# Kernel optimization log

Measured on AMD Instinct MI355X. Metric: run time of the kernel, lower is better.

The kernel has to match this reference:

```python
import jax, jax.numpy as jnp
import numpy as np

SR = 24000
N_FFT = 1024
N_MELS = 128
FMIN = 0.0
LPC_ORDER = 4
REPEAT = 256
F0 = 40.0
CLAMP = 1e-12
T_FRAMES = 16384


def _hz_to_mel(f):
    # librosa slaney scale
    f = np.asarray(f, dtype=np.float64)
    f_sp = 200.0 / 3
    min_log_hz = 1000.0
    min_log_mel = min_log_hz / f_sp
    logstep = np.log(6.4) / 27.0
    mels = f / f_sp
    log_t = f >= min_log_hz
    mels = np.where(log_t, min_log_mel + np.log(np.maximum(f, min_log_hz) / min_log_hz) / logstep, mels)
    return mels


def _mel_to_hz(m):
    m = np.asarray(m, dtype=np.float64)
    f_sp = 200.0 / 3
    min_log_hz = 1000.0
    min_log_mel = min_log_hz / f_sp
    logstep = np.log(6.4) / 27.0
    freqs = f_sp * m
    log_t = m >= min_log_mel
    freqs = np.where(log_t, min_log_hz * np.exp(logstep * (m - min_log_mel)), freqs)
    return freqs


def librosa_mel_fn(sr, n_fft, n_mels, fmin, fmax):
    if fmax is None:
        fmax = sr / 2.0
    fftfreqs = np.linspace(0.0, sr / 2.0, n_fft // 2 + 1)
    mel_f = _mel_to_hz(np.linspace(_hz_to_mel(fmin), _hz_to_mel(fmax), n_mels + 2))
    fdiff = np.diff(mel_f)
    ramps = mel_f[:, None] - fftfreqs[None, :]
    lower = -ramps[:-2] / fdiff[:-1, None]
    upper = ramps[2:] / fdiff[1:, None]
    weights = np.maximum(0.0, np.minimum(lower, upper))
    enorm = 2.0 / (mel_f[2 : n_mels + 2] - mel_f[:n_mels])  # slaney norm
    weights *= enorm[:, None]
    return weights.astype(np.float32)


def setup_inputs() -> dict:
    key = jax.random.key(0)
    mel = jax.random.normal(key, (1, N_MELS, T_FRAMES), dtype=jnp.float32)
    mel_basis = librosa_mel_fn(SR, N_FFT, N_MELS, FMIN, None)  # [128, 513]
    inv_mel_basis = jnp.asarray(np.linalg.pinv(mel_basis), dtype=jnp.float32)  # [513, 128]
    theta = (2.0 * np.pi * F0 / SR) ** 2
    lag_window = jnp.asarray(
        np.exp(-0.5 * theta * np.arange(LPC_ORDER + 1, dtype=np.float32) ** 2)[:, None],
        dtype=jnp.float32,
    )  # [lpc_order+1, 1]
    return {"mel": mel, "inv_mel_basis": inv_mel_basis, "lag_window": lag_window}


def _levinson_durbin(AC, n):
    # AC: [n+1, T] autocorrelation; returns LPC coeffs [n, T]
    E = AC[0]
    lp = []  # list of [T]
    for i in range(n):
        acc = AC[i + 1]
        for j in range(i):
            acc = acc + lp[j] * AC[i - j]
        ki = acc / E
        c = jnp.maximum(1.0 - ki * ki, 1e-5)
        E = E * c
        lp = [lp[j] - ki * lp[i - j - 1] for j in range(i)] + [-ki]
    return jnp.stack(lp, axis=0)  # [n, T]


def reference(mel, inv_mel_basis, lag_window):
    # mel: [1, n_mel, T]
    mel_lin = jnp.power(10.0, mel)
    linear = jnp.maximum(jnp.einsum("fm,bmt->bft", inv_mel_basis, mel_lin), CLAMP)  # [1, 513, T]
    power = linear ** 2
    flipped = jnp.flip(power, axis=1)[:, 1:-1, :]
    fft_power = jnp.concatenate([power, flipped], axis=1)  # [1, n_fft, T]
    auto_corr = jnp.fft.ifft(fft_power, axis=1).real[:, : LPC_ORDER + 1, :]  # [1, n+1, T]
    auto_corr = auto_corr * lag_window[None, :, :]
    lpc = _levinson_durbin(auto_corr[0], LPC_ORDER)[None]  # [1, n, T]
    lpc_ctrl = -jnp.flip(lpc, axis=1)
    lpc_ctrl = jnp.repeat(lpc_ctrl, REPEAT, axis=-1)  # [1, n, T*repeat]
    return lpc_ctrl
```

## Files before the change

### kernel.cpp

```cpp
#include <hip/hip_runtime.h>

#define T_FRAMES 16384
#define N_MELS 128
#define N_FREQ 513
#define FPB 64
#define BT 512
#define LOG2_10 3.3219280948873623f

typedef short bf16x8 __attribute__((ext_vector_type(8)));
typedef unsigned short u16x8 __attribute__((ext_vector_type(8)));
typedef float f32x4 __attribute__((ext_vector_type(4)));

__device__ __forceinline__ unsigned short f2bf(float x) {
  unsigned u = __float_as_uint(x);
  return (unsigned short)((u + 0x7FFFu + ((u >> 16) & 1u)) >> 16);
}
__device__ __forceinline__ float bf2f(unsigned short h) {
  return __uint_as_float(((unsigned)h) << 16);
}

__global__ __launch_bounds__(256) void build_bimg(
    const float* __restrict__ B, unsigned short* __restrict__ img) {
  int gid = blockIdx.x * 256 + threadIdx.x;
  int l  = gid & 63;
  int hl = (gid >> 6) & 1;
  int ks = (gid >> 7) & 3;
  int ft = (gid >> 9) & 3;
  int w  = gid >> 11;
  int f  = w * 64 + ft * 16 + (l & 15);
  int k0 = ks * 32 + (l >> 4) * 8;
  const float* src = B + f * N_MELS + k0;
  u16x8 o;
#pragma unroll
  for (int j = 0; j < 8; ++j) {
    float x = src[j];
    unsigned short hi = f2bf(x);
    o[j] = hl ? f2bf(x - bf2f(hi)) : hi;
  }
  *((u16x8*)img + gid) = o;
}

__global__ __launch_bounds__(BT, 2) void mel2lpc_mfma(
    const float* __restrict__ mel,
    const float* __restrict__ B,
    const float* __restrict__ lag,
    const unsigned short* __restrict__ bimg,
    float* __restrict__ lpcw)
{
  __shared__ float X32T[64][132];
  __shared__ __align__(16) short Xf[32][512];
  __shared__ float W_s[5][N_FREQ];
  __shared__ float red[8][5][64];

  const int tid = threadIdx.x;
  const int lane = tid & 63;
  const int w = __builtin_amdgcn_readfirstlane(tid >> 6);
  const int t0 = blockIdx.x * FPB;

  for (int idx = tid; idx < 5 * N_FREQ; idx += BT) {
    int k = idx / N_FREQ;
    int f = idx - k * N_FREQ;
    float cf = (f == 0 || f == N_FREQ - 1) ? (1.0f / 1024.0f) : (2.0f / 1024.0f);
    W_s[k][f] = lag[k] * cf * cospif((float)(k * f) * (1.0f / 512.0f));
  }
#pragma unroll
  for (int r = 0; r < 16; ++r) {
    int idx = r * BT + tid;
    int t = idx & 63;
    int m = idx >> 6;
    X32T[t][m] = exp2f(mel[m * T_FRAMES + t0 + t] * LOG2_10);
  }
  __syncthreads();

#pragma unroll
  for (int pi = 0; pi < 2; ++pi) {
    int pr = w * 2 + pi;
    int tt = pr >> 2, ks = pr & 3;
    int t = tt * 16 + (lane & 15);
    int k0 = ks * 32 + (lane >> 4) * 8;
    float4 a0 = *(const float4*)&X32T[t][k0];
    float4 a1 = *(const float4*)&X32T[t][k0 + 4];
    float xs[8] = {a0.x, a0.y, a0.z, a0.w, a1.x, a1.y, a1.z, a1.w};
    u16x8 vh, vl;
#pragma unroll
    for (int j = 0; j < 8; ++j) {
      unsigned short hi = f2bf(xs[j]);
      vh[j] = hi;
      vl[j] = f2bf(xs[j] - bf2f(hi));
    }
    int fi = (tt * 4 + ks) * 2;
    *(u16x8*)&Xf[fi][lane * 8] = vh;
    *(u16x8*)&Xf[fi + 1][lane * 8] = vl;
  }
  __syncthreads();

  f32x4 acc[4][4];
#pragma unroll
  for (int ft = 0; ft < 4; ++ft)
#pragma unroll
    for (int tt = 0; tt < 4; ++tt) acc[ft][tt] = (f32x4){0.f, 0.f, 0.f, 0.f};

  const bf16x8* bfr = (const bf16x8*)bimg;
#pragma unroll
  for (int ks = 0; ks < 4; ++ks) {
    bf16x8 xh[4], xl[4], ah[4], al[4];
#pragma unroll
    for (int tt = 0; tt < 4; ++tt) {
      xh[tt] = *(const bf16x8*)&Xf[(tt * 4 + ks) * 2][lane * 8];
      xl[tt] = *(const bf16x8*)&Xf[(tt * 4 + ks) * 2 + 1][lane * 8];
    }
#pragma unroll
    for (int ft = 0; ft < 4; ++ft) {
      int fr = ((w * 4 + ft) * 4 + ks) * 2;
      ah[ft] = bfr[fr * 64 + lane];
      al[ft] = bfr[(fr + 1) * 64 + lane];
    }
#pragma unroll
    for (int ft = 0; ft < 4; ++ft)
#pragma unroll
      for (int tt = 0; tt < 4; ++tt) {
        acc[ft][tt] = __builtin_amdgcn_mfma_f32_16x16x32_bf16(ah[ft], xh[tt], acc[ft][tt], 0, 0, 0);
        acc[ft][tt] = __builtin_amdgcn_mfma_f32_16x16x32_bf16(ah[ft], xl[tt], acc[ft][tt], 0, 0, 0);
        acc[ft][tt] = __builtin_amdgcn_mfma_f32_16x16x32_bf16(al[ft], xh[tt], acc[ft][tt], 0, 0, 0);
      }
  }

  float pk[5][4];
#pragma unroll
  for (int k = 0; k < 5; ++k)
#pragma unroll
    for (int tt = 0; tt < 4; ++tt) pk[k][tt] = 0.f;

#pragma unroll
  for (int ft = 0; ft < 4; ++ft) {
#pragma unroll
    for (int j = 0; j < 4; ++j) {
      int f = w * 64 + ft * 16 + ((lane >> 4) << 2) + j;
      float w0 = W_s[0][f], w1 = W_s[1][f], w2 = W_s[2][f];
      float w3 = W_s[3][f], w4 = W_s[4][f];
#pragma unroll
      for (int tt = 0; tt < 4; ++tt) {
        float lin = fmaxf(acc[ft][tt][j], 1e-12f);
        float p = lin * lin;
        pk[0][tt] = fmaf(w0, p, pk[0][tt]);
        pk[1][tt] = fmaf(w1, p, pk[1][tt]);
        pk[2][tt] = fmaf(w2, p, pk[2][tt]);
        pk[3][tt] = fmaf(w3, p, pk[3][tt]);
        pk[4][tt] = fmaf(w4, p, pk[4][tt]);
      }
    }
  }
#pragma unroll
  for (int k = 0; k < 5; ++k)
#pragma unroll
    for (int tt = 0; tt < 4; ++tt) {
      float v = pk[k][tt];
      v += __shfl_xor(v, 16);
      v += __shfl_xor(v, 32);
      if (lane < 16) red[w][k][tt * 16 + lane] = v;
    }
  __syncthreads();

  if (tid < 64) {
    const int t = tid;
    float ac[5];
#pragma unroll
    for (int k = 0; k < 5; ++k) {
      float s = 0.f;
#pragma unroll
      for (int w2 = 0; w2 < 8; ++w2) s += red[w2][k][t];
      ac[k] = s;
    }
    float s = 0.f;
    const float4* __restrict__ B512 = (const float4*)(B + 512 * N_MELS);
#pragma unroll
    for (int mi = 0; mi < 32; ++mi) {
      float4 b = B512[mi];
      float4 xv = *(const float4*)&X32T[t][mi * 4];
      s = fmaf(b.x, xv.x, s); s = fmaf(b.y, xv.y, s);
      s = fmaf(b.z, xv.z, s); s = fmaf(b.w, xv.w, s);
    }
    float lin = fmaxf(s, 1e-12f);
    float pv = lin * lin;
#pragma unroll
    for (int k = 0; k < 5; ++k) ac[k] = fmaf(W_s[k][512], pv, ac[k]);

    float E = ac[0];
    float k0 = ac[1] / E;
    E *= fmaxf(1.0f - k0 * k0, 1e-5f);
    float l0 = -k0;

    float a1 = ac[2] + l0 * ac[1];
    float k1 = a1 / E;
    E *= fmaxf(1.0f - k1 * k1, 1e-5f);
    float m0 = l0 - k1 * l0;
    float m1 = -k1;

    float a2 = ac[3] + m0 * ac[2] + m1 * ac[1];
    float k2 = a2 / E;
    E *= fmaxf(1.0f - k2 * k2, 1e-5f);
    float n0 = m0 - k2 * m1;
    float n1 = m1 - k2 * m0;
    float n2 = -k2;

    float a3 = ac[4] + n0 * ac[3] + n1 * ac[2] + n2 * ac[1];
    float k3 = a3 / E;
    float o0 = n0 - k3 * n2;
    float o1 = n1 - k3 * n1;
    float o2 = n2 - k3 * n0;
    float o3 = -k3;

    lpcw[0 * T_FRAMES + t0 + t] = -o3;
    lpcw[1 * T_FRAMES + t0 + t] = -o2;
    lpcw[2 * T_FRAMES + t0 + t] = -o1;
    lpcw[3 * T_FRAMES + t0 + t] = -o0;
  }
}

__global__ __launch_bounds__(256) void expand(
    const float* __restrict__ lpc, float4* __restrict__ out4) {
  int g = blockIdx.x * 2048 + threadIdx.x;
#pragma unroll
  for (int i = 0; i < 8; ++i) {
    int gi = g + i * 256;
    int j = gi >> 20;
    int rem = gi & 1048575;
    int frame = rem >> 6;
    float v = lpc[j * T_FRAMES + frame];
    out4[gi] = make_float4(v, v, v, v);
  }
}

extern "C" void kernel_launch(void* const* d_in, const int* in_sizes, int n_in,
                              void* d_out, int out_size, void* d_ws, size_t ws_size,
                              hipStream_t stream) {
  const float* mel = (const float*)d_in[0];
  const float* B   = (const float*)d_in[1];
  const float* lag = (const float*)d_in[2];
  float* ws = (float*)d_ws;
  unsigned short* bimg = (unsigned short*)ws;
  float* lpcw = ws + 65536;
  build_bimg<<<64, 256, 0, stream>>>(B, bimg);
  mel2lpc_mfma<<<T_FRAMES / FPB, BT, 0, stream>>>(mel, B, lag, bimg, lpcw);
  expand<<<2048, 256, 0, stream>>>(lpcw, (float4*)d_out);
}
```

Before: 97.53 us.

## Fuse repeat-expansion into mel2lpc kernel and halve frames per block

Removes the separate expand kernel: each block now writes its repeated LPC output (4 x 32 frames x 256) directly from shared memory, so the intermediate LPC workspace round trip and one launch go away. Frames per block drop from 64 to 32, shared memory is overlaid into one aliased buffer, and launch bounds are raised to allow 4 blocks per SM, which doubles the grid and raises occupancy. The bin-512 dot product moves earlier so it runs alongside the bf16 split. In exchange, each block reloads the bf16 B image for half as many frames, which doubles B traffic per frame.

```diff
diff --git a/kernel.cpp b/kernel.cpp
--- a/kernel.cpp
+++ b/kernel.cpp
@@ -3,7 +3,7 @@
 #define T_FRAMES 16384
 #define N_MELS 128
 #define N_FREQ 513
-#define FPB 64
+#define FPB 32
 #define BT 512
 #define LOG2_10 3.3219280948873623f
 
@@ -40,42 +40,67 @@
   *((u16x8*)img + gid) = o;
 }
 
-__global__ __launch_bounds__(BT, 2) void mel2lpc_mfma(
+#define SM_X32T 0
+#define SM_RED  0
+#define SM_LP   5120
+#define SM_XF   16896
+#define SM_W    33280
+#define SM_PV   43552
+#define SM_SIZE 43712
+
+__global__ __launch_bounds__(BT, 4) void mel2lpc_mfma(
     const float* __restrict__ mel,
     const float* __restrict__ B,
     const float* __restrict__ lag,
     const unsigned short* __restrict__ bimg,
-    float* __restrict__ lpcw)
+    float* __restrict__ out)
 {
-  __shared__ float X32T[64][132];
-  __shared__ __align__(16) short Xf[32][512];
-  __shared__ float W_s[5][N_FREQ];
-  __shared__ float red[8][5][64];
+  __shared__ __align__(16) char smem[SM_SIZE];
+  float (*X32T)[132] = (float(*)[132])(smem + SM_X32T);
+  short (*Xf)[512]   = (short(*)[512])(smem + SM_XF);
+  float (*W_s)[513]  = (float(*)[513])(smem + SM_W);
+  float (*red)[5][32] = (float(*)[5][32])(smem + SM_RED);
+  float (*lp)[32]    = (float(*)[32])(smem + SM_LP);
+  float* pv512       = (float*)(smem + SM_PV);
 
   const int tid = threadIdx.x;
   const int lane = tid & 63;
   const int w = __builtin_amdgcn_readfirstlane(tid >> 6);
   const int t0 = blockIdx.x * FPB;
 
-  for (int idx = tid; idx < 5 * N_FREQ; idx += BT) {
-    int k = idx / N_FREQ;
-    int f = idx - k * N_FREQ;
-    float cf = (f == 0 || f == N_FREQ - 1) ? (1.0f / 1024.0f) : (2.0f / 1024.0f);
-    W_s[k][f] = lag[k] * cf * cospif((float)(k * f) * (1.0f / 512.0f));
-  }
-#pragma unroll
-  for (int r = 0; r < 16; ++r) {
+#pragma unroll
+  for (int k = 0; k < 5; ++k) {
+    float lk = lag[k];
+    for (int f = tid; f < N_FREQ; f += BT) {
+      float cf = (f == 0 || f == N_FREQ - 1) ? (1.0f / 1024.0f) : (2.0f / 1024.0f);
+      W_s[k][f] = lk * cf * cospif((float)(k * f) * (1.0f / 512.0f));
+    }
+  }
+#pragma unroll
+  for (int r = 0; r < 8; ++r) {
     int idx = r * BT + tid;
-    int t = idx & 63;
-    int m = idx >> 6;
+    int t = idx & 31;
+    int m = idx >> 5;
     X32T[t][m] = exp2f(mel[m * T_FRAMES + t0 + t] * LOG2_10);
   }
   __syncthreads();
 
-#pragma unroll
-  for (int pi = 0; pi < 2; ++pi) {
-    int pr = w * 2 + pi;
-    int tt = pr >> 2, ks = pr & 3;
+  if (tid < FPB) {
+    const int t = tid;
+    float s = 0.f;
+    const float4* __restrict__ B512 = (const float4*)(B + 512 * N_MELS);
+#pragma unroll
+    for (int mi = 0; mi < 32; ++mi) {
+      float4 b = B512[mi];
+      float4 xv = *(const float4*)&X32T[t][mi * 4];
+      s = fmaf(b.x, xv.x, s); s = fmaf(b.y, xv.y, s);
+      s = fmaf(b.z, xv.z, s); s = fmaf(b.w, xv.w, s);
+    }
+    float lin = fmaxf(s, 1e-12f);
+    pv512[t] = lin * lin;
+  }
+  {
+    int tt = w >> 2, ks = w & 3;
     int t = tt * 16 + (lane & 15);
     int k0 = ks * 32 + (lane >> 4) * 8;
     float4 a0 = *(const float4*)&X32T[t][k0];
@@ -88,48 +113,43 @@
       vh[j] = hi;
       vl[j] = f2bf(xs[j] - bf2f(hi));
     }
-    int fi = (tt * 4 + ks) * 2;
-    *(u16x8*)&Xf[fi][lane * 8] = vh;
-    *(u16x8*)&Xf[fi + 1][lane * 8] = vl;
-  }
-  __syncthreads();
-
-  f32x4 acc[4][4];
+    *(u16x8*)&Xf[w * 2][lane * 8] = vh;
+    *(u16x8*)&Xf[w * 2 + 1][lane * 8] = vl;
+  }
+  __syncthreads();
+
+  f32x4 acc[4][2];
 #pragma unroll
   for (int ft = 0; ft < 4; ++ft)
 #pragma unroll
-    for (int tt = 0; tt < 4; ++tt) acc[ft][tt] = (f32x4){0.f, 0.f, 0.f, 0.f};
+    for (int tt = 0; tt < 2; ++tt) acc[ft][tt] = (f32x4){0.f, 0.f, 0.f, 0.f};
 
   const bf16x8* bfr = (const bf16x8*)bimg;
 #pragma unroll
   for (int ks = 0; ks < 4; ++ks) {
-    bf16x8 xh[4], xl[4], ah[4], al[4];
-#pragma unroll
-    for (int tt = 0; tt < 4; ++tt) {
-      xh[tt] = *(const bf16x8*)&Xf[(tt * 4 + ks) * 2][lane * 8];
-      xl[tt] = *(const bf16x8*)&Xf[(tt * 4 + ks) * 2 + 1][lane * 8];
-    }
+    bf16x8 xh0 = *(const bf16x8*)&Xf[(0 * 4 + ks) * 2][lane * 8];
+    bf16x8 xl0 = *(const bf16x8*)&Xf[(0 * 4 + ks) * 2 + 1][lane * 8];
+    bf16x8 xh1 = *(const bf16x8*)&Xf[(1 * 4 + ks) * 2][lane * 8];
+    bf16x8 xl1 = *(const bf16x8*)&Xf[(1 * 4 + ks) * 2 + 1][lane * 8];
 #pragma unroll
     for (int ft = 0; ft < 4; ++ft) {
       int fr = ((w * 4 + ft) * 4 + ks) * 2;
-      ah[ft] = bfr[fr * 64 + lane];
-      al[ft] = bfr[(fr + 1) * 64 + lane];
-    }
-#pragma unroll
-    for (int ft = 0; ft < 4; ++ft)
-#pragma unroll
-      for (int tt = 0; tt < 4; ++tt) {
-        acc[ft][tt] = __builtin_amdgcn_mfma_f32_16x16x32_bf16(ah[ft], xh[tt], acc[ft][tt], 0, 0, 0);
-        acc[ft][tt] = __builtin_amdgcn_mfma_f32_16x16x32_bf16(ah[ft], xl[tt], acc[ft][tt], 0, 0, 0);
-        acc[ft][tt] = __builtin_amdgcn_mfma_f32_16x16x32_bf16(al[ft], xh[tt], acc[ft][tt], 0, 0, 0);
-      }
-  }
-
-  float pk[5][4];
+      bf16x8 ah = bfr[fr * 64 + lane];
+      bf16x8 al = bfr[(fr + 1) * 64 + lane];
+      acc[ft][0] = __builtin_amdgcn_mfma_f32_16x16x32_bf16(ah, xh0, acc[ft][0], 0, 0, 0);
+      acc[ft][0] = __builtin_amdgcn_mfma_f32_16x16x32_bf16(ah, xl0, acc[ft][0], 0, 0, 0);
+      acc[ft][0] = __builtin_amdgcn_mfma_f32_16x16x32_bf16(al, xh0, acc[ft][0], 0, 0, 0);
+      acc[ft][1] = __builtin_amdgcn_mfma_f32_16x16x32_bf16(ah, xh1, acc[ft][1], 0, 0, 0);
+      acc[ft][1] = __builtin_amdgcn_mfma_f32_16x16x32_bf16(ah, xl1, acc[ft][1], 0, 0, 0);
+      acc[ft][1] = __builtin_amdgcn_mfma_f32_16x16x32_bf16(al, xh1, acc[ft][1], 0, 0, 0);
+    }
+  }
+
+  float pk[5][2];
 #pragma unroll
   for (int k = 0; k < 5; ++k)
 #pragma unroll
-    for (int tt = 0; tt < 4; ++tt) pk[k][tt] = 0.f;
+    for (int tt = 0; tt < 2; ++tt) pk[k][tt] = 0.f;
 
 #pragma unroll
   for (int ft = 0; ft < 4; ++ft) {
@@ -139,7 +159,7 @@
       float w0 = W_s[0][f], w1 = W_s[1][f], w2 = W_s[2][f];
       float w3 = W_s[3][f], w4 = W_s[4][f];
 #pragma unroll
-      for (int tt = 0; tt < 4; ++tt) {
+      for (int tt = 0; tt < 2; ++tt) {
         float lin = fmaxf(acc[ft][tt][j], 1e-12f);
         float p = lin * lin;
         pk[0][tt] = fmaf(w0, p, pk[0][tt]);
@@ -153,7 +173,7 @@
 #pragma unroll
   for (int k = 0; k < 5; ++k)
 #pragma unroll
-    for (int tt = 0; tt < 4; ++tt) {
+    for (int tt = 0; tt < 2; ++tt) {
       float v = pk[k][tt];
       v += __shfl_xor(v, 16);
       v += __shfl_xor(v, 32);
@@ -161,7 +181,7 @@
     }
   __syncthreads();
 
-  if (tid < 64) {
+  if (tid < FPB) {
     const int t = tid;
     float ac[5];
 #pragma unroll
@@ -169,21 +189,8 @@
       float s = 0.f;
 #pragma unroll
       for (int w2 = 0; w2 < 8; ++w2) s += red[w2][k][t];
-      ac[k] = s;
-    }
-    float s = 0.f;
-    const float4* __restrict__ B512 = (const float4*)(B + 512 * N_MELS);
-#pragma unroll
-    for (int mi = 0; mi < 32; ++mi) {
-      float4 b = B512[mi];
-      float4 xv = *(const float4*)&X32T[t][mi * 4];
-      s = fmaf(b.x, xv.x, s); s = fmaf(b.y, xv.y, s);
-      s = fmaf(b.z, xv.z, s); s = fmaf(b.w, xv.w, s);
-    }
-    float lin = fmaxf(s, 1e-12f);
-    float pv = lin * lin;
-#pragma unroll
-    for (int k = 0; k < 5; ++k) ac[k] = fmaf(W_s[k][512], pv, ac[k]);
+      ac[k] = s + W_s[k][512] * pv512[t];
+    }
 
     float E = ac[0];
     float k0 = ac[1] / E;
@@ -210,24 +217,23 @@
     float o2 = n2 - k3 * n0;
     float o3 = -k3;
 
-    lpcw[0 * T_FRAMES + t0 + t] = -o3;
-    lpcw[1 * T_FRAMES + t0 + t] = -o2;
-    lpcw[2 * T_FRAMES + t0 + t] = -o1;
-    lpcw[3 * T_FRAMES + t0 + t] = -o0;
-  }
-}
-
-__global__ __launch_bounds__(256) void expand(
-    const float* __restrict__ lpc, float4* __restrict__ out4) {
-  int g = blockIdx.x * 2048 + threadIdx.x;
-#pragma unroll
-  for (int i = 0; i < 8; ++i) {
-    int gi = g + i * 256;
-    int j = gi >> 20;
-    int rem = gi & 1048575;
-    int frame = rem >> 6;
-    float v = lpc[j * T_FRAMES + frame];
-    out4[gi] = make_float4(v, v, v, v);
+    lp[0][t] = -o3;
+    lp[1][t] = -o2;
+    lp[2][t] = -o1;
+    lp[3][t] = -o0;
+  }
+  __syncthreads();
+
+  float4* out4 = (float4*)out;
+#pragma unroll
+  for (int i = 0; i < 16; ++i) {
+    int vid = i * BT + tid;
+    int j = vid >> 11;
+    int rem = vid & 2047;
+    int tl = rem >> 6;
+    float v = lp[j][tl];
+    out4[(size_t)j * (T_FRAMES * 256 / 4) + (size_t)t0 * 64 + rem] =
+        make_float4(v, v, v, v);
   }
 }
 
@@ -237,10 +243,7 @@
   const float* mel = (const float*)d_in[0];
   const float* B   = (const float*)d_in[1];
   const float* lag = (const float*)d_in[2];
-  float* ws = (float*)d_ws;
-  unsigned short* bimg = (unsigned short*)ws;
-  float* lpcw = ws + 65536;
+  unsigned short* bimg = (unsigned short*)d_ws;
   build_bimg<<<64, 256, 0, stream>>>(B, bimg);
-  mel2lpc_mfma<<<T_FRAMES / FPB, BT, 0, stream>>>(mel, B, lag, bimg, lpcw);
-  expand<<<2048, 256, 0, stream>>>(lpcw, (float4*)d_out);
-}
+  mel2lpc_mfma<<<T_FRAMES / FPB, BT, 0, stream>>>(mel, B, lag, bimg, (float*)d_out);
+}
```

Measured after the change: 94.85 us. -2.8%, faster.
